# Performance work log

Hardware: AMD Instinct MI355X
Metric: run time of the kernel (lower is better)

The kernel has to match this reference:

```python
import jax, jax.numpy as jnp
import numpy as np

KH, KW = 3, 3
STRIDE = 1
OUT_C = 512


def im2col(x, kh, kw, stride):
    # x: [N, C, H, W] -> col: [C*kh*kw, N*oh*ow]  (row order: C major, then kh, kw)
    N, C, H, W = x.shape
    oh = (H - kh) // stride + 1
    ow = (W - kw) // stride + 1
    rows = jnp.arange(oh)[:, None] * stride + jnp.arange(kh)[None, :]  # [oh, kh]
    cols = jnp.arange(ow)[:, None] * stride + jnp.arange(kw)[None, :]  # [ow, kw]
    # gather windows: result [N, C, oh, kh, ow, kw]
    A = x[:, :, rows[:, :, None, None], cols[None, None, :, :]]
    # permute to (C, kh, kw, N, oh, ow) then flatten, matching torch permute(1,4,5,0,2,3)
    col = jnp.transpose(A, (1, 3, 5, 0, 2, 4)).reshape(C * kh * kw, N * oh * ow)
    return col, oh, ow


def setup_inputs() -> dict:
    key = jax.random.key(0)
    k1, k2, k3 = jax.random.split(key, 3)
    N, C, H, W = 16, 256, 32, 32
    K_sel = (C * KH * KW) // 2  # 1152 rows kept by the binary mask
    x = jax.random.normal(k1, (N, C, H, W), dtype=jnp.float32)
    weight = jax.random.normal(k2, (K_sel, OUT_C), dtype=jnp.float32) * 0.02
    idx = jnp.sort(jax.random.randint(k3, (K_sel,), 0, C * KH * KW, dtype=jnp.int32))
    return {"x": x, "weight": weight, "idx": idx}


def reference(x, weight, idx):
    N = x.shape[0]
    col, oh, ow = im2col(x, KH, KW, STRIDE)          # [C*kh*kw, N*oh*ow]
    x_tile = col[idx, :].T                            # gather masked rows -> [N*oh*ow, K_sel]
    conv_out = x_tile @ weight                        # [N*oh*ow, out_c]
    conv_out = conv_out.reshape(N, oh * ow, OUT_C)
    conv_out = jnp.transpose(conv_out, (0, 2, 1)).reshape(N, OUT_C, oh, ow)
    return conv_out
```

## Files before the change

### kernel.cpp

```cpp
#include <hip/hip_runtime.h>
#include <stdint.h>

#define N_IMG   16
#define C_IN    256
#define H_IN    32
#define W_IN    32
#define OH      30
#define OW      30
#define K_SEL   1152
#define OUTC    512
#define RY_TOT  (N_IMG * OH)
#define M_HAT   (RY_TOT * 32)
#define X_ELEMS (N_IMG * C_IN * H_IN * W_IN)
#define OUT_SP  (OH * OW)
#define CHW     (C_IN * H_IN * W_IN)

#define TO      128
#define TM      64
#define NMT     (M_HAT / TM)
#define NOT     (OUTC / TO)
#define BSTR    40
#define KITER   (K_SEL / 32)

typedef float f32x4  __attribute__((ext_vector_type(4)));
typedef short bf16x8 __attribute__((ext_vector_type(8)));

__device__ __forceinline__ unsigned short f2bf(float f) {
    unsigned int u = __float_as_uint(f);
    u += 0x7FFFu + ((u >> 16) & 1u);
    return (unsigned short)(u >> 16);
}

__device__ __forceinline__ void gl_lds16(const void* g, void* lds) {
    __builtin_amdgcn_global_load_lds(
        (const __attribute__((address_space(1))) unsigned int*)g,
        (__attribute__((address_space(3))) unsigned int*)lds,
        16, 0, 0);
}

__global__ void prep_kernel(const int* __restrict__ idx, const float* __restrict__ w,
                            int* __restrict__ koff, unsigned short* __restrict__ wT) {
    __shared__ float tile[32][33];
    const int bx = blockIdx.x, by = blockIdx.y, t = threadIdx.x;

    if (by == 0) {
        int k = bx * 256 + t;
        if (k < K_SEL) {
            int v = idx[k];
            int c = v / 9, rem = v - c * 9;
            int i = rem / 3, j = rem - i * 3;
            koff[k] = c * (H_IN * W_IN) + i * W_IN + j;
        }
    }
    const int s0 = bx * 32, o0 = by * 32;
    const int oc = t & 31, sg = t >> 5;
#pragma unroll
    for (int i = 0; i < 4; ++i) {
        int sl = sg * 4 + i;
        tile[sl][oc] = w[(s0 + sl) * OUTC + o0 + oc];
    }
    __syncthreads();
    const int ol = t >> 3, sq = t & 7;
    unsigned int u0 = (unsigned int)f2bf(tile[sq * 4 + 0][ol]) |
                      ((unsigned int)f2bf(tile[sq * 4 + 1][ol]) << 16);
    unsigned int u1 = (unsigned int)f2bf(tile[sq * 4 + 2][ol]) |
                      ((unsigned int)f2bf(tile[sq * 4 + 3][ol]) << 16);
    uint2 pk; pk.x = u0; pk.y = u1;
    *reinterpret_cast<uint2*>(&wT[(size_t)(o0 + ol) * K_SEL + s0 + sq * 4]) = pk;
}

__global__ __launch_bounds__(256, 4)
void gemm_kernel(const unsigned short* __restrict__ wT, const float* __restrict__ x,
                 const int* __restrict__ koff, float* __restrict__ out) {
    __shared__ __align__(16) unsigned short As[TO * 32];
    __shared__ __align__(16) unsigned short Bs[4][TM * BSTR];
    __shared__ int koS[K_SEL];

    const int t    = threadIdx.x;
    const int wave = t >> 6;
    const int lane = t & 63;
    const int quad = lane >> 4;
    const int lo   = lane & 15;

    const int bid = blockIdx.x;
    const int mt  = bid % NMT;
    const int ot  = bid / NMT;
    const int oBase = ot * TO;
    const int mBase = mt * TM;

    for (int i = t; i < K_SEL; i += 256) koS[i] = koff[i];

    const int xw  = t & 31;
    const int xwc = min(xw, 29);
    int basex[2];
#pragma unroll
    for (int ry = 0; ry < 2; ++ry) {
        int ryg = mt * 2 + ry;
        int n = ryg / 30, y = ryg - n * 30;
        basex[ry] = n * CHW + y * W_IN + xwc;
    }

    const int kq4 = t >> 5;
    const int ks  = kq4 * 4;

    const int lrow = lane >> 2, csw = (lane & 3) ^ ((lrow >> 1) & 3);
    const unsigned short* wrow0 = wT + (size_t)(oBase + wave * 32 + lrow) * K_SEL + csw * 8;
    const unsigned short* wrow1 = wT + (size_t)(oBase + wave * 32 + 16 + lrow) * K_SEL + csw * 8;
    unsigned short* lA0 = &As[(wave * 32) * 32];
    unsigned short* lA1 = lA0 + 16 * 32;

    const int aswz = quad ^ ((lo >> 1) & 3);
    const unsigned short* aB = &As[(wave * 32 + lo) * 32 + aswz * 8];
    const unsigned short* bB[4] = {
        &Bs[0][lo * BSTR + quad * 8], &Bs[1][lo * BSTR + quad * 8],
        &Bs[2][lo * BSTR + quad * 8], &Bs[3][lo * BSTR + quad * 8] };
    unsigned short* bW[4] = {
        &Bs[0][xw * BSTR + ks], &Bs[1][xw * BSTR + ks],
        &Bs[2][xw * BSTR + ks], &Bs[3][xw * BSTR + ks] };

    __syncthreads();

    f32x4 acc[2][4] = {};
    float v[2][2][4];

    gl_lds16(wrow0, lA0);
    gl_lds16(wrow1, lA1);
#pragma unroll
    for (int tl = 0; tl < 2; ++tl) {
        int4 k4 = *(const int4*)&koS[tl * 32 + ks];
#pragma unroll
        for (int ry = 0; ry < 2; ++ry)
#pragma unroll
            for (int j = 0; j < 4; ++j)
                v[tl][ry][j] = x[basex[ry] + ((const int*)&k4)[j]];
    }
    asm volatile("s_waitcnt vmcnt(8)" ::: "memory");
#pragma unroll
    for (int ry = 0; ry < 2; ++ry) {
        unsigned int u0 = (unsigned int)f2bf(v[0][ry][0]) |
                          ((unsigned int)f2bf(v[0][ry][1]) << 16);
        unsigned int u1 = (unsigned int)f2bf(v[0][ry][2]) |
                          ((unsigned int)f2bf(v[0][ry][3]) << 16);
        uint2 pk; pk.x = u0; pk.y = u1;
        *reinterpret_cast<uint2*>(bW[0] + ry * 32 * BSTR) = pk;
    }
    {
        int4 k4 = *(const int4*)&koS[2 * 32 + ks];
#pragma unroll
        for (int ry = 0; ry < 2; ++ry)
#pragma unroll
            for (int j = 0; j < 4; ++j)
                v[0][ry][j] = x[basex[ry] + ((const int*)&k4)[j]];
    }
    asm volatile("s_waitcnt vmcnt(8)" ::: "memory");
#pragma unroll
    for (int ry = 0; ry < 2; ++ry) {
        unsigned int u0 = (unsigned int)f2bf(v[1][ry][0]) |
                          ((unsigned int)f2bf(v[1][ry][1]) << 16);
        unsigned int u1 = (unsigned int)f2bf(v[1][ry][2]) |
                          ((unsigned int)f2bf(v[1][ry][3]) << 16);
        uint2 pk; pk.x = u0; pk.y = u1;
        *reinterpret_cast<uint2*>(bW[1] + ry * 32 * BSTR) = pk;
    }
    asm volatile("s_waitcnt lgkmcnt(0)" ::: "memory");
    __builtin_amdgcn_s_barrier();

#define KSTEP(KT, C, VR, VW) do {                                              \
    asm volatile("s_waitcnt vmcnt(8)" ::: "memory");        \
    bf16x8 a0_ = *(const bf16x8*)(aB);                                         \
    bf16x8 a1_ = *(const bf16x8*)(aB + 16 * 32);                               \
    bf16x8 b0_ = *(const bf16x8*)(bB[C]);                                      \
    bf16x8 b1_ = *(const bf16x8*)(bB[C] + 16 * BSTR);                          \
    bf16x8 b2_ = *(const bf16x8*)(bB[C] + 32 * BSTR);                          \
    bf16x8 b3_ = *(const bf16x8*)(bB[C] + 48 * BSTR);                          \
    const int kg_ = ((KT) + 3 < KITER ? (KT) + 3 : KITER - 1) * 32;            \
    int4 k4_ = *(const int4*)&koS[kg_ + ks];                                   \
    asm volatile("s_waitcnt lgkmcnt(0)" ::: "memory");   \
    __builtin_amdgcn_sched_barrier(0);                                         \
    const int k1_ = ((KT) + 1 < KITER ? (KT) + 1 : KITER - 1) * 32;            \
    gl_lds16(wrow0 + k1_, lA0);                         \
    gl_lds16(wrow1 + k1_, lA1);                                                \
    _Pragma("unroll")                                                          \
    for (int ry = 0; ry < 2; ++ry)                                             \
        _Pragma("unroll")                                                      \
        for (int j = 0; j < 4; ++j)                                            \
            v[VW][ry][j] = x[basex[ry] + ((const int*)&k4_)[j]];               \
    asm volatile("s_waitcnt vmcnt(10)" ::: "memory");   \
    _Pragma("unroll")                                                          \
    for (int ry = 0; ry < 2; ++ry) {                                           \
        unsigned int u0_ = (unsigned int)f2bf(v[VR][ry][0]) |                  \
                           ((unsigned int)f2bf(v[VR][ry][1]) << 16);           \
        unsigned int u1_ = (unsigned int)f2bf(v[VR][ry][2]) |                  \
                           ((unsigned int)f2bf(v[VR][ry][3]) << 16);           \
        uint2 pk_; pk_.x = u0_; pk_.y = u1_;                                   \
        *reinterpret_cast<uint2*>(bW[((C) + 2) & 3] + ry * 32 * BSTR) = pk_;   \
    }                                                                          \
    __builtin_amdgcn_s_setprio(1);                                             \
    acc[0][0] = __builtin_amdgcn_mfma_f32_16x16x32_bf16(a0_, b0_, acc[0][0], 0, 0, 0); \
    acc[0][1] = __builtin_amdgcn_mfma_f32_16x16x32_bf16(a0_, b1_, acc[0][1], 0, 0, 0); \
    acc[0][2] = __builtin_amdgcn_mfma_f32_16x16x32_bf16(a0_, b2_, acc[0][2], 0, 0, 0); \
    acc[0][3] = __builtin_amdgcn_mfma_f32_16x16x32_bf16(a0_, b3_, acc[0][3], 0, 0, 0); \
    acc[1][0] = __builtin_amdgcn_mfma_f32_16x16x32_bf16(a1_, b0_, acc[1][0], 0, 0, 0); \
    acc[1][1] = __builtin_amdgcn_mfma_f32_16x16x32_bf16(a1_, b1_, acc[1][1], 0, 0, 0); \
    acc[1][2] = __builtin_amdgcn_mfma_f32_16x16x32_bf16(a1_, b2_, acc[1][2], 0, 0, 0); \
    acc[1][3] = __builtin_amdgcn_mfma_f32_16x16x32_bf16(a1_, b3_, acc[1][3], 0, 0, 0); \
    __builtin_amdgcn_s_setprio(0);                                             \
} while (0)

    for (int kt0 = 0; kt0 < KITER; kt0 += 4) {
        KSTEP(kt0 + 0, 0, 0, 1);
        KSTEP(kt0 + 1, 1, 1, 0);
        asm volatile("s_waitcnt lgkmcnt(0)" ::: "memory");
        __builtin_amdgcn_s_barrier();
        KSTEP(kt0 + 2, 2, 0, 1);
        KSTEP(kt0 + 3, 3, 1, 0);
        asm volatile("s_waitcnt lgkmcnt(0)" ::: "memory");
        __builtin_amdgcn_s_barrier();
    }
#undef KSTEP

#pragma unroll
    for (int ns = 0; ns < 4; ++ns) {
        const int mh  = mBase + ns * 16 + lo;
        const int xwe = mh & 31;
        const int ryg = mh >> 5;
        const int n = ryg / 30, y = ryg - n * 30;
        if (xwe < OW) {
            const size_t ob = (size_t)n * (OUTC * OUT_SP) + (size_t)y * OW + xwe;
#pragma unroll
            for (int ms = 0; ms < 2; ++ms) {
                const int o0 = oBase + wave * 32 + ms * 16 + quad * 4;
#pragma unroll
                for (int r = 0; r < 4; ++r)
                    out[ob + (size_t)(o0 + r) * OUT_SP] = acc[ms][ns][r];
            }
        }
    }
}

extern "C" void kernel_launch(void* const* d_in, const int* in_sizes, int n_in,
                              void* d_out, int out_size, void* d_ws, size_t ws_size,
                              hipStream_t stream) {
    const float* x   = (const float*)d_in[0];
    const float* w   = (const float*)d_in[1];
    const int*   idx = (const int*)d_in[2];
    float*       out = (float*)d_out;

    char* ws = (char*)d_ws;
    int*            koff = (int*)ws;
    unsigned short* wT   = (unsigned short*)(ws + 4608);

    prep_kernel<<<dim3(K_SEL / 32, OUTC / 32), dim3(256), 0, stream>>>(idx, w, koff, wT);
    gemm_kernel<<<dim3(NMT * NOT), dim3(256), 0, stream>>>(wT, x, koff, out);
}
```

Before: 122.0 us.

## Deepen x-gather prefetch to four register slots and remap block order by image

Extends the register prefetch of gathered x values from two slots to four, so each gather is issued two k-steps ahead of its pack into LDS. This gives global gather latency more time to hide behind the MFMA work. Separately, block indices are remapped so neighbouring blocks work on the same image and output tile, which should improve L2 reuse of x and weights. It costs more VGPRs per thread, which may reduce occupancy under launch_bounds(256,4), and the fixed vmcnt wait counts now have to match the new ordering of outstanding loads.

Result: slower. 131.0 us (+7.4%).

```diff
diff --git a/kernel.cpp b/kernel.cpp
--- a/kernel.cpp
+++ b/kernel.cpp
@@ -83,8 +83,13 @@
     const int lo   = lane & 15;
 
     const int bid = blockIdx.x;
-    const int mt  = bid % NMT;
-    const int ot  = bid / NMT;
+    const int g   = bid & 7;
+    const int h   = bid >> 3;
+    const int nimg = g + 8 * (h & 1);
+    const int h2  = h >> 1;
+    const int mtl = h2 % 15;
+    const int ot  = h2 / 15;
+    const int mt  = nimg * 15 + mtl;
     const int oBase = ot * TO;
     const int mBase = mt * TM;
 
@@ -104,8 +109,10 @@
     const int ks  = kq4 * 4;
 
     const int lrow = lane >> 2, csw = (lane & 3) ^ ((lrow >> 1) & 3);
-    const unsigned short* wrow0 = wT + (size_t)(oBase + wave * 32 + lrow) * K_SEL + csw * 8;
-    const unsigned short* wrow1 = wT + (size_t)(oBase + wave * 32 + 16 + lrow) * K_SEL + csw * 8;
+    const unsigned short* wrow0 =
+        wT + (size_t)(oBase + wave * 32 + lrow) * K_SEL + csw * 8;
+    const unsigned short* wrow1 =
+        wT + (size_t)(oBase + wave * 32 + 16 + lrow) * K_SEL + csw * 8;
     unsigned short* lA0 = &As[(wave * 32) * 32];
     unsigned short* lA1 = lA0 + 16 * 32;
 
@@ -121,80 +128,57 @@
     __syncthreads();
 
     f32x4 acc[2][4] = {};
-    float v[2][2][4];
-
+    float v[4][2][4];
+
+#define GATHER(TL, SLOT) do {                                                  \
+    int4 k4 = *(const int4*)&koS[(TL) * 32 + ks];                              \
+    _Pragma("unroll")                                                          \
+    for (int ry = 0; ry < 2; ++ry)                                             \
+        _Pragma("unroll")                                                      \
+        for (int j = 0; j < 4; ++j)                                            \
+            v[SLOT][ry][j] = x[basex[ry] + ((const int*)&k4)[j]];              \
+} while (0)
+
+#define PACK(SLOT, DST) do {                                                   \
+    _Pragma("unroll")                                                          \
+    for (int ry = 0; ry < 2; ++ry) {                                           \
+        unsigned int u0_ = (unsigned int)f2bf(v[SLOT][ry][0]) |                \
+                           ((unsigned int)f2bf(v[SLOT][ry][1]) << 16);         \
+        unsigned int u1_ = (unsigned int)f2bf(v[SLOT][ry][2]) |                \
+                           ((unsigned int)f2bf(v[SLOT][ry][3]) << 16);         \
+        uint2 pk_; pk_.x = u0_; pk_.y = u1_;                                   \
+        *reinterpret_cast<uint2*>(bW[DST] + ry * 32 * BSTR) = pk_;             \
+    }                                                                          \
+} while (0)
+
+    GATHER(0, 0);
+    GATHER(1, 1);
+    asm volatile("s_waitcnt vmcnt(8)" ::: "memory");
+    PACK(0, 0);
+    asm volatile("s_waitcnt vmcnt(0)" ::: "memory");
+    PACK(1, 1);
+    GATHER(2, 2);
     gl_lds16(wrow0, lA0);
     gl_lds16(wrow1, lA1);
-#pragma unroll
-    for (int tl = 0; tl < 2; ++tl) {
-        int4 k4 = *(const int4*)&koS[tl * 32 + ks];
-#pragma unroll
-        for (int ry = 0; ry < 2; ++ry)
-#pragma unroll
-            for (int j = 0; j < 4; ++j)
-                v[tl][ry][j] = x[basex[ry] + ((const int*)&k4)[j]];
-    }
-    asm volatile("s_waitcnt vmcnt(8)" ::: "memory");
-#pragma unroll
-    for (int ry = 0; ry < 2; ++ry) {
-        unsigned int u0 = (unsigned int)f2bf(v[0][ry][0]) |
-                          ((unsigned int)f2bf(v[0][ry][1]) << 16);
-        unsigned int u1 = (unsigned int)f2bf(v[0][ry][2]) |
-                          ((unsigned int)f2bf(v[0][ry][3]) << 16);
-        uint2 pk; pk.x = u0; pk.y = u1;
-        *reinterpret_cast<uint2*>(bW[0] + ry * 32 * BSTR) = pk;
-    }
-    {
-        int4 k4 = *(const int4*)&koS[2 * 32 + ks];
-#pragma unroll
-        for (int ry = 0; ry < 2; ++ry)
-#pragma unroll
-            for (int j = 0; j < 4; ++j)
-                v[0][ry][j] = x[basex[ry] + ((const int*)&k4)[j]];
-    }
-    asm volatile("s_waitcnt vmcnt(8)" ::: "memory");
-#pragma unroll
-    for (int ry = 0; ry < 2; ++ry) {
-        unsigned int u0 = (unsigned int)f2bf(v[1][ry][0]) |
-                          ((unsigned int)f2bf(v[1][ry][1]) << 16);
-        unsigned int u1 = (unsigned int)f2bf(v[1][ry][2]) |
-                          ((unsigned int)f2bf(v[1][ry][3]) << 16);
-        uint2 pk; pk.x = u0; pk.y = u1;
-        *reinterpret_cast<uint2*>(bW[1] + ry * 32 * BSTR) = pk;
-    }
+    GATHER(3, 3);
     asm volatile("s_waitcnt lgkmcnt(0)" ::: "memory");
     __builtin_amdgcn_s_barrier();
 
-#define KSTEP(KT, C, VR, VW) do {                                              \
-    asm volatile("s_waitcnt vmcnt(8)" ::: "memory");        \
+#define KSTEP(KT, C) do {                                                      \
+    asm volatile("s_waitcnt vmcnt(8)" ::: "memory");                           \
     bf16x8 a0_ = *(const bf16x8*)(aB);                                         \
     bf16x8 a1_ = *(const bf16x8*)(aB + 16 * 32);                               \
     bf16x8 b0_ = *(const bf16x8*)(bB[C]);                                      \
     bf16x8 b1_ = *(const bf16x8*)(bB[C] + 16 * BSTR);                          \
     bf16x8 b2_ = *(const bf16x8*)(bB[C] + 32 * BSTR);                          \
     bf16x8 b3_ = *(const bf16x8*)(bB[C] + 48 * BSTR);                          \
-    const int kg_ = ((KT) + 3 < KITER ? (KT) + 3 : KITER - 1) * 32;            \
-    int4 k4_ = *(const int4*)&koS[kg_ + ks];                                   \
-    asm volatile("s_waitcnt lgkmcnt(0)" ::: "memory");   \
+    asm volatile("s_waitcnt lgkmcnt(0)" ::: "memory");      \
     __builtin_amdgcn_sched_barrier(0);                                         \
     const int k1_ = ((KT) + 1 < KITER ? (KT) + 1 : KITER - 1) * 32;            \
     gl_lds16(wrow0 + k1_, lA0);                         \
     gl_lds16(wrow1 + k1_, lA1);                                                \
-    _Pragma("unroll")                                                          \
-    for (int ry = 0; ry < 2; ++ry)                                             \
-        _Pragma("unroll")                                                      \
-        for (int j = 0; j < 4; ++j)                                            \
-            v[VW][ry][j] = x[basex[ry] + ((const int*)&k4_)[j]];               \
-    asm volatile("s_waitcnt vmcnt(10)" ::: "memory");   \
-    _Pragma("unroll")                                                          \
-    for (int ry = 0; ry < 2; ++ry) {                                           \
-        unsigned int u0_ = (unsigned int)f2bf(v[VR][ry][0]) |                  \
-                           ((unsigned int)f2bf(v[VR][ry][1]) << 16);           \
-        unsigned int u1_ = (unsigned int)f2bf(v[VR][ry][2]) |                  \
-                           ((unsigned int)f2bf(v[VR][ry][3]) << 16);           \
-        uint2 pk_; pk_.x = u0_; pk_.y = u1_;                                   \
-        *reinterpret_cast<uint2*>(bW[((C) + 2) & 3] + ry * 32 * BSTR) = pk_;   \
-    }                                                                          \
+    GATHER(((KT) + 4 < KITER ? (KT) + 4 : KITER - 1), C);                      \
+    PACK((C + 2) & 3, (C + 2) & 3);                       \
     __builtin_amdgcn_s_setprio(1);                                             \
     acc[0][0] = __builtin_amdgcn_mfma_f32_16x16x32_bf16(a0_, b0_, acc[0][0], 0, 0, 0); \
     acc[0][1] = __builtin_amdgcn_mfma_f32_16x16x32_bf16(a0_, b1_, acc[0][1], 0, 0, 0); \
@@ -208,16 +192,18 @@
 } while (0)
 
     for (int kt0 = 0; kt0 < KITER; kt0 += 4) {
-        KSTEP(kt0 + 0, 0, 0, 1);
-        KSTEP(kt0 + 1, 1, 1, 0);
+        KSTEP(kt0 + 0, 0);
+        KSTEP(kt0 + 1, 1);
         asm volatile("s_waitcnt lgkmcnt(0)" ::: "memory");
         __builtin_amdgcn_s_barrier();
-        KSTEP(kt0 + 2, 2, 0, 1);
-        KSTEP(kt0 + 3, 3, 1, 0);
+        KSTEP(kt0 + 2, 2);
+        KSTEP(kt0 + 3, 3);
         asm volatile("s_waitcnt lgkmcnt(0)" ::: "memory");
         __builtin_amdgcn_s_barrier();
     }
 #undef KSTEP
+#undef GATHER
+#undef PACK
 
 #pragma unroll
     for (int ns = 0; ns < 4; ++ns) {
```
